# Performance work log

Measured on AMD Instinct MI355X. Metric: run time of the kernel, lower is better.

The kernel has to match this reference:

```python
import jax, jax.numpy as jnp
import numpy as np

EPS = 1e-5  # torch BatchNorm2d default eps

def _bn(x, gamma, beta):
    # training-mode batch statistics over (N,H,W), per channel (biased variance)
    mean = jnp.mean(x, axis=(0, 2, 3), keepdims=True)
    var = jnp.var(x, axis=(0, 2, 3), keepdims=True)
    return gamma[None, :, None, None] * (x - mean) * jax.lax.rsqrt(var + EPS) + beta[None, :, None, None]

def _conv1x1(x, w, b):
    # (B,C,H,W) x (O,C) -> (B,O,H,W)
    return jnp.einsum('bchw,oc->bohw', x, w) + b[None, :, None, None]

def _maxpool2(x):
    B, C, H, W = x.shape
    return x.reshape(B, C, H // 2, 2, W // 2, 2).max(axis=(3, 5))

def setup_inputs() -> dict:
    key = jax.random.key(0)
    ks = jax.random.split(key, 5)
    B, C, H, W = 16, 256, 56, 56
    Ci, Cg = C // 8, C // 4
    def kaiming(k, o, i):
        return jax.random.normal(k, (o, i), jnp.float32) * np.float32(np.sqrt(2.0 / i))
    return {
        'x': jax.random.normal(ks[0], (B, C, H, W), jnp.float32),
        'bn1_gamma': jnp.ones((C,), jnp.float32),
        'bn1_beta': jnp.zeros((C,), jnp.float32),
        'w_g': kaiming(ks[1], Cg, C), 'b_g': jnp.zeros((Cg,), jnp.float32),
        'w_theta': kaiming(ks[2], Ci, C), 'b_theta': jnp.zeros((Ci,), jnp.float32),
        'w_phi': kaiming(ks[3], Ci, C), 'b_phi': jnp.zeros((Ci,), jnp.float32),
        'bn2_gamma': jnp.ones((Cg,), jnp.float32),
        'bn2_beta': jnp.zeros((Cg,), jnp.float32),
        'w_z': kaiming(ks[4], C, Cg), 'b_z': jnp.zeros((C,), jnp.float32),
    }

def reference(x, bn1_gamma, bn1_beta, w_g, b_g, w_theta, b_theta, w_phi, b_phi, bn2_gamma, bn2_beta, w_z, b_z):
    identity = x
    B, C, H, W = x.shape
    xa = jax.nn.relu(_bn(x, bn1_gamma, bn1_beta))
    g_x = _maxpool2(_conv1x1(xa, w_g, b_g))        # (B,Cg,H/2,W/2)
    phi_x = _maxpool2(_conv1x1(xa, w_phi, b_phi))  # (B,Ci,H/2,W/2)
    theta_x = _conv1x1(xa, w_theta, b_theta)       # (B,Ci,H,W)
    Cg = g_x.shape[1]
    Ci = theta_x.shape[1]
    Np = g_x.shape[2] * g_x.shape[3]               # subsampled positions (H/2*W/2)
    g_x = g_x.reshape(B, Cg, Np).transpose(0, 2, 1)      # (B,Np,Cg)
    phi_x = phi_x.reshape(B, Ci, Np)                     # (B,Ci,Np)
    theta_x = theta_x.reshape(B, Ci, H * W).transpose(0, 2, 1)  # (B,HW,Ci)
    f_div_C = jnp.einsum('bnc,bcm->bnm', theta_x, phi_x) / Np   # (B,HW,Np)
    y = jnp.einsum('bnm,bmc->bnc', f_div_C, g_x)                # (B,HW,Cg)
    y = y.transpose(0, 2, 1).reshape(B, Cg, H, W)
    w_y = _conv1x1(jax.nn.relu(_bn(y, bn2_gamma, bn2_beta)), w_z, b_z)
    return w_y + identity
```

## Files before the change

### kernel.cpp

```cpp
#include <hip/hip_runtime.h>
#include <hip/hip_bf16.h>

#define BB 16
#define CC 256
#define HWN 3136
#define NCG 64
#define NCI 32
#define NPP 784

typedef __attribute__((ext_vector_type(8))) short short8;
typedef __attribute__((ext_vector_type(4))) float floatx4;

__device__ __forceinline__ unsigned short f2bf(float f) {
    union { __hip_bfloat16 h; unsigned short u; } cv;
    cv.h = __float2bfloat16(f);
    return cv.u;
}
__device__ __forceinline__ float bf2f(unsigned short u) {
    return __uint_as_float(((unsigned)u) << 16);
}

__global__ __launch_bounds__(256) void k_prep(const float* __restrict__ w_t,
                                              const float* __restrict__ w_p,
                                              const float* __restrict__ w_g,
                                              const float* __restrict__ w_z,
                                              unsigned short* __restrict__ wcat,
                                              unsigned short* __restrict__ wzb,
                                              unsigned short* __restrict__ pool,
                                              float* __restrict__ accs) {
    int o = blockIdx.x;
    int c = threadIdx.x;
    const float* src = (o < 32) ? (w_t + o * CC)
                      : (o < 64) ? (w_p + (o - 32) * CC)
                                 : (w_g + (o - 64) * CC);
    wcat[o * CC + c] = f2bf(src[c]);
    {
        int r = o * 2 + (c >> 7);
        int kk = c & 127;
        if (kk < 72)
            wzb[r * 72 + kk] = (kk < 64) ? f2bf(w_z[r * 64 + kk]) : (unsigned short)0;
    }
    if (o < 96) {
        int b = c >> 4, kk = c & 15;
        pool[((size_t)(b * 96 + o)) * 800 + 784 + kk] = 0;
    }
    if (o == 0) {
        for (int i = c; i < 1152; i += 256) accs[i] = 0.f;
    }
}

__global__ __launch_bounds__(256) void k_bn1a(const float* __restrict__ x,
                                              float* __restrict__ acc) {
    int blk = blockIdx.x;
    int c = blk & (CC - 1);
    const float4* p = (const float4*)(x + (size_t)blk * HWN);
    int tid = threadIdx.x;
    float s = 0.f, q = 0.f;
    #pragma unroll
    for (int i = tid; i < 784; i += 256) {
        float4 v = p[i];
        s += v.x + v.y + v.z + v.w;
        q += v.x * v.x + v.y * v.y + v.z * v.z + v.w * v.w;
    }
    #pragma unroll
    for (int off = 32; off > 0; off >>= 1) {
        s += __shfl_down(s, off);
        q += __shfl_down(q, off);
    }
    __shared__ float sh[8];
    int wid = tid >> 6, lane = tid & 63;
    if (lane == 0) { sh[wid] = s; sh[4 + wid] = q; }
    __syncthreads();
    if (tid == 0) {
        atomicAdd(&acc[c], sh[0] + sh[1] + sh[2] + sh[3]);
        atomicAdd(&acc[CC + c], sh[4] + sh[5] + sh[6] + sh[7]);
    }
}

__global__ __launch_bounds__(256) void k_conv1(const float* __restrict__ x,
                                               const unsigned short* __restrict__ wcat,
                                               const float* __restrict__ bn1acc,
                                               const float* __restrict__ gamma,
                                               const float* __restrict__ beta,
                                               const float* __restrict__ b_g,
                                               const float* __restrict__ b_t,
                                               const float* __restrict__ b_p,
                                               unsigned short* __restrict__ th,
                                               unsigned short* __restrict__ pool,
                                               float* __restrict__ T1g) {
    int b  = blockIdx.y;
    int bx = blockIdx.x;
    int hw0 = bx * 112;
    int tid = threadIdx.x;
    int wv = tid >> 6, ln = tid & 63;
    int col = ln & 15, quad = ln >> 4;

    __shared__ unsigned short smem[128 * 120];
    unsigned short* As = smem;
    unsigned short* Bs = smem + 4096;
    __shared__ float ab_s[512];
    __shared__ float bias_s[128];

    {
        const float inv = 1.0f / (BB * HWN);
        float mean = bn1acc[tid] * inv;
        float var  = bn1acc[CC + tid] * inv - mean * mean;
        float a = gamma[tid] * rsqrtf(var + 1e-5f);
        ab_s[tid] = a;
        ab_s[CC + tid] = beta[tid] - mean * a;
    }
    if (tid < 128) {
        int o = tid;
        bias_s[o] = (o < 32) ? b_t[o] : (o < 64) ? b_p[o - 32] : b_g[o - 64];
    }
    __syncthreads();

    floatx4 acc[2][7];
    #pragma unroll
    for (int mt = 0; mt < 2; ++mt)
        for (int nt = 0; nt < 7; ++nt)
            acc[mt][nt] = (floatx4){0.f, 0.f, 0.f, 0.f};

    int p   = tid & 15;
    int hwq = tid >> 4;
    const float* xb = x + (size_t)(b * CC) * HWN + hw0;
    bool q1 = (hwq + 16) < 28;

    float4 pv0[2], pv1[2];
    {
        int c0 = 2 * p;
        pv0[0] = *(const float4*)(xb + (size_t)c0 * HWN + hwq * 4);
        pv1[0] = *(const float4*)(xb + (size_t)(c0 + 1) * HWN + hwq * 4);
        if (q1) {
            pv0[1] = *(const float4*)(xb + (size_t)c0 * HWN + (hwq + 16) * 4);
            pv1[1] = *(const float4*)(xb + (size_t)(c0 + 1) * HWN + (hwq + 16) * 4);
        }
    }

    for (int k0 = 0; k0 < CC; k0 += 32) {
        #pragma unroll
        for (int i = 0; i < 2; ++i) {
            int row = wv * 32 + i * 16 + (ln >> 2);
            int q   = ln & 3;
            const unsigned short* gp = wcat + row * CC + k0 + q * 8;
            __builtin_amdgcn_global_load_lds(
                (const __attribute__((address_space(1))) unsigned int*)gp,
                (__attribute__((address_space(3))) unsigned int*)&As[(wv * 2 + i) * 512],
                16, 0, 0);
        }
        {
            int c0 = k0 + 2 * p;
            float a0 = ab_s[c0],     d0 = ab_s[CC + c0];
            float a1 = ab_s[c0 + 1], d1 = ab_s[CC + c0 + 1];
            unsigned int* bw = (unsigned int*)Bs;
            #pragma unroll
            for (int t = 0; t < 2; ++t) {
                if (t == 0 || q1) {
                    int qi = hwq + 16 * t;
                    float4 v0 = pv0[t], v1 = pv1[t];
                    float r0[4] = { fmaxf(fmaf(a0, v0.x, d0), 0.f), fmaxf(fmaf(a0, v0.y, d0), 0.f),
                                    fmaxf(fmaf(a0, v0.z, d0), 0.f), fmaxf(fmaf(a0, v0.w, d0), 0.f) };
                    float r1[4] = { fmaxf(fmaf(a1, v1.x, d1), 0.f), fmaxf(fmaf(a1, v1.y, d1), 0.f),
                                    fmaxf(fmaf(a1, v1.z, d1), 0.f), fmaxf(fmaf(a1, v1.w, d1), 0.f) };
                    #pragma unroll
                    for (int i = 0; i < 4; ++i) {
                        unsigned int w = (unsigned int)f2bf(r0[i]) | ((unsigned int)f2bf(r1[i]) << 16);
                        bw[(qi * 4 + i) * 16 + p] = w;
                    }
                }
            }
        }
        if (k0 + 32 < CC) {
            int c0 = k0 + 32 + 2 * p;
            pv0[0] = *(const float4*)(xb + (size_t)c0 * HWN + hwq * 4);
            pv1[0] = *(const float4*)(xb + (size_t)(c0 + 1) * HWN + hwq * 4);
            if (q1) {
                pv0[1] = *(const float4*)(xb + (size_t)c0 * HWN + (hwq + 16) * 4);
                pv1[1] = *(const float4*)(xb + (size_t)(c0 + 1) * HWN + (hwq + 16) * 4);
            }
        }
        __syncthreads();

        short8 af0 = *(const short8*)&As[(wv * 32 +      col) * 32 + quad * 8];
        short8 af1 = *(const short8*)&As[(wv * 32 + 16 + col) * 32 + quad * 8];
        #pragma unroll
        for (int nt = 0; nt < 7; ++nt) {
            short8 bf = *(const short8*)&Bs[(nt * 16 + col) * 32 + quad * 8];
            acc[0][nt] = __builtin_amdgcn_mfma_f32_16x16x32_bf16(af0, bf, acc[0][nt], 0, 0, 0);
            acc[1][nt] = __builtin_amdgcn_mfma_f32_16x16x32_bf16(af1, bf, acc[1][nt], 0, 0, 0);
        }
        __syncthreads();
    }

    unsigned short* Ct = smem;
    #pragma unroll
    for (int mt = 0; mt < 2; ++mt) {
        int obase = wv * 32 + mt * 16 + quad * 4;
        #pragma unroll
        for (int r = 0; r < 4; ++r) {
            float bias = bias_s[obase + r];
            #pragma unroll
            for (int nt = 0; nt < 7; ++nt)
                Ct[(obase + r) * 120 + nt * 16 + col] = f2bf(acc[mt][nt][r] + bias);
        }
    }
    __syncthreads();

    #pragma unroll
    for (int i = 0; i < 4; ++i) {
        int e = tid + i * 256;
        if (e < 896) {
            int ch = e / 28, c4 = e - ch * 28;
            ushort4 v = *(const ushort4*)&Ct[ch * 120 + c4 * 4];
            *(ushort4*)&th[((size_t)(b * NCI + ch)) * HWN + hw0 + c4 * 4] = v;
        }
    }
    {
        int row = tid >> 3;
        int seg = tid & 7;
        float s = 0.f;
        #pragma unroll
        for (int j = 0; j < 14; ++j) s += bf2f(Ct[row * 120 + seg * 14 + j]);
        s += __shfl_down(s, 4);
        s += __shfl_down(s, 2);
        s += __shfl_down(s, 1);
        if (seg == 0) atomicAdd(&T1g[b * NCI + row], s);
    }
    #pragma unroll
    for (int i = 0; i < 11; ++i) {
        int e = tid + i * 256;
        if (e < 2688) {
            int ch = e / 28, m = e - ch * 28;
            const unsigned short* r0p = &Ct[(32 + ch) * 120 + 2 * m];
            float v = fmaxf(fmaxf(bf2f(r0p[0]), bf2f(r0p[1])),
                            fmaxf(bf2f(r0p[56]), bf2f(r0p[57])));
            pool[((size_t)(b * 96 + ch)) * 800 + bx * 28 + m] = f2bf(v);
        }
    }
}

__global__ __launch_bounds__(512) void k_sgemm(const unsigned short* __restrict__ pool,
                                               const unsigned short* __restrict__ th,
                                               const float* __restrict__ T1g,
                                               unsigned short* __restrict__ Sg,
                                               float* __restrict__ bn2acc) {
    int b = blockIdx.x;
    int tid = threadIdx.x;
    int wv = tid >> 6, ln = tid & 63;
    int col = ln & 15, quad = ln >> 4;
    __shared__ float Sred[4 * 2048];
    __shared__ float Gred[4 * 1024];
    __shared__ float T1s[32];
    __shared__ float shs[64], shq[64];

    if (tid < 64) { shs[tid] = 0.f; shq[tid] = 0.f; }
    if (tid < 32) T1s[tid] = T1g[b * NCI + tid];

    if (wv < 4) {
        const unsigned short* gbase = pool + ((size_t)(b * 96 + 32)) * 800;
        const unsigned short* pbase = pool + ((size_t)(b * 96)) * 800;
        floatx4 acc[4][2];
        #pragma unroll
        for (int mt = 0; mt < 4; ++mt)
            for (int nt = 0; nt < 2; ++nt)
                acc[mt][nt] = (floatx4){0.f, 0.f, 0.f, 0.f};
        for (int s = wv; s < 25; s += 4) {
            int k0 = s * 32;
            short8 af[4], bfr[2];
            #pragma unroll
            for (int mt = 0; mt < 4; ++mt)
                af[mt] = *(const short8*)&gbase[(mt * 16 + col) * 800 + k0 + quad * 8];
            #pragma unroll
            for (int nt = 0; nt < 2; ++nt)
                bfr[nt] = *(const short8*)&pbase[(nt * 16 + col) * 800 + k0 + quad * 8];
            #pragma unroll
            for (int mt = 0; mt < 4; ++mt)
                #pragma unroll
                for (int nt = 0; nt < 2; ++nt)
                    acc[mt][nt] = __builtin_amdgcn_mfma_f32_16x16x32_bf16(af[mt], bfr[nt], acc[mt][nt], 0, 0, 0);
        }
        #pragma unroll
        for (int mt = 0; mt < 4; ++mt)
            for (int nt = 0; nt < 2; ++nt)
                for (int r = 0; r < 4; ++r) {
                    int cg = mt * 16 + quad * 4 + r;
                    int ci = nt * 16 + col;
                    Sred[wv * 2048 + cg * 32 + ci] = acc[mt][nt][r];
                }
    } else {
        int gw = wv - 4;
        const unsigned short* tb = th + (size_t)(b * NCI) * HWN;
        floatx4 ga[2][2];
        #pragma unroll
        for (int m = 0; m < 2; ++m)
            for (int n = 0; n < 2; ++n)
                ga[m][n] = (floatx4){0.f, 0.f, 0.f, 0.f};
        for (int t = gw; t < 98; t += 4) {
            int k0 = t * 32;
            short8 a0 = *(const short8*)&tb[(size_t)col * HWN + k0 + quad * 8];
            short8 a1 = *(const short8*)&tb[(size_t)(16 + col) * HWN + k0 + quad * 8];
            ga[0][0] = __builtin_amdgcn_mfma_f32_16x16x32_bf16(a0, a0, ga[0][0], 0, 0, 0);
            ga[0][1] = __builtin_amdgcn_mfma_f32_16x16x32_bf16(a0, a1, ga[0][1], 0, 0, 0);
            ga[1][0] = __builtin_amdgcn_mfma_f32_16x16x32_bf16(a1, a0, ga[1][0], 0, 0, 0);
            ga[1][1] = __builtin_amdgcn_mfma_f32_16x16x32_bf16(a1, a1, ga[1][1], 0, 0, 0);
        }
        #pragma unroll
        for (int m = 0; m < 2; ++m)
            for (int n = 0; n < 2; ++n)
                for (int r = 0; r < 4; ++r)
                    Gred[gw * 1024 + (m * 16 + quad * 4 + r) * 32 + n * 16 + col] = ga[m][n][r];
    }
    __syncthreads();

    for (int idx = tid; idx < 2048; idx += 512) {
        float s = Sred[idx] + Sred[2048 + idx] + Sred[4096 + idx] + Sred[6144 + idx];
        int cg = idx >> 5, ci = idx & 31;
        unsigned short h = f2bf(s * (1.0f / NPP));
        Sg[(size_t)b * 2560 + cg * 40 + ci] = h;
        Sred[idx] = bf2f(h);
    }
    for (int idx = tid; idx < 1024; idx += 512) {
        Gred[idx] = Gred[idx] + Gred[1024 + idx] + Gred[2048 + idx] + Gred[3072 + idx];
    }
    __syncthreads();

    {
        int cg = tid & 63, part = tid >> 6;
        float sum = 0.f, sq = 0.f;
        #pragma unroll
        for (int i = 0; i < 4; ++i) {
            int ci = part * 4 + i;
            float sv = Sred[cg * 32 + ci];
            sum += sv * T1s[ci];
            float t = 0.f;
            #pragma unroll
            for (int cj = 0; cj < 32; ++cj)
                t += Gred[ci * 32 + cj] * Sred[cg * 32 + cj];
            sq += sv * t;
        }
        atomicAdd(&shs[cg], sum);
        atomicAdd(&shq[cg], sq);
    }
    __syncthreads();
    if (tid < 64) {
        atomicAdd(&bn2acc[tid], shs[tid]);
        atomicAdd(&bn2acc[64 + tid], shq[tid]);
    }
}

__global__ __launch_bounds__(256) void k_convz(const unsigned short* __restrict__ th,
                                               const unsigned short* __restrict__ Sg,
                                               const unsigned short* __restrict__ wzb,
                                               const float* __restrict__ bn2acc,
                                               const float* __restrict__ gamma,
                                               const float* __restrict__ beta,
                                               const float* __restrict__ b_z,
                                               const float* __restrict__ x,
                                               float* __restrict__ out) {
    int b = blockIdx.y;
    int hw0 = blockIdx.x * 64;
    int coh = blockIdx.z * 128;
    int tid = threadIdx.x;
    int wv = tid >> 6, ln = tid & 63;
    int col = ln & 15, quad = ln >> 4;

    __shared__ unsigned short Wl[128 * 72];
    __shared__ unsigned short TS[5120];
    __shared__ float ab2_s[128];
    unsigned short* Tt = TS;
    unsigned short* St = TS + 2560;
    unsigned short* Yt = TS;

    for (int j = wv; j < 18; j += 4) {
        const unsigned short* gp = wzb + coh * 72 + j * 512 + ln * 8;
        __builtin_amdgcn_global_load_lds(
            (const __attribute__((address_space(1))) unsigned int*)gp,
            (__attribute__((address_space(3))) unsigned int*)&Wl[j * 512],
            16, 0, 0);
    }
    if (tid < 64) {
        const float inv = 1.0f / (BB * HWN);
        float mean = bn2acc[tid] * inv;
        float var  = bn2acc[64 + tid] * inv - mean * mean;
        float a = gamma[tid] * rsqrtf(var + 1e-5f);
        ab2_s[tid] = a;
        ab2_s[64 + tid] = beta[tid] - mean * a;
    }
    {
        const unsigned int* sgw = (const unsigned int*)(Sg + (size_t)b * 2560);
        unsigned int* stw = (unsigned int*)St;
        for (int i = tid; i < 1280; i += 256) stw[i] = sgw[i];
    }
    {
        int p2 = tid & 15, hwq = tid >> 4;
        int c0 = 2 * p2;
        const unsigned short* tb = th + (size_t)(b * NCI) * HWN + hw0 + hwq * 4;
        ushort4 v0 = *(const ushort4*)(tb + (size_t)c0 * HWN);
        ushort4 v1 = *(const ushort4*)(tb + (size_t)(c0 + 1) * HWN);
        unsigned int* tw = (unsigned int*)Tt;
        tw[(hwq * 4 + 0) * 20 + p2] = (unsigned)v0.x | ((unsigned)v1.x << 16);
        tw[(hwq * 4 + 1) * 20 + p2] = (unsigned)v0.y | ((unsigned)v1.y << 16);
        tw[(hwq * 4 + 2) * 20 + p2] = (unsigned)v0.z | ((unsigned)v1.z << 16);
        tw[(hwq * 4 + 3) * 20 + p2] = (unsigned)v0.w | ((unsigned)v1.w << 16);
    }
    __syncthreads();

    short8 afy = *(const short8*)&Tt[(wv * 16 + col) * 40 + quad * 8];
    floatx4 yacc[4];
    #pragma unroll
    for (int nt = 0; nt < 4; ++nt) {
        short8 bf = *(const short8*)&St[(nt * 16 + col) * 40 + quad * 8];
        floatx4 z = (floatx4){0.f, 0.f, 0.f, 0.f};
        yacc[nt] = __builtin_amdgcn_mfma_f32_16x16x32_bf16(afy, bf, z, 0, 0, 0);
    }
    __syncthreads();

    #pragma unroll
    for (int nt = 0; nt < 4; ++nt) {
        int cg = nt * 16 + col;
        float a = ab2_s[cg], d = ab2_s[64 + cg];
        #pragma unroll
        for (int r = 0; r < 4; ++r) {
            int hwl = wv * 16 + quad * 4 + r;
            Yt[hwl * 72 + cg] = f2bf(fmaxf(fmaf(a, yacc[nt][r], d), 0.f));
        }
    }
    __syncthreads();

    floatx4 acc[8];
    #pragma unroll
    for (int nt = 0; nt < 8; ++nt) acc[nt] = (floatx4){0.f, 0.f, 0.f, 0.f};

    #pragma unroll
    for (int kk = 0; kk < 2; ++kk) {
        short8 afm = *(const short8*)&Yt[(wv * 16 + col) * 72 + kk * 32 + quad * 8];
        #pragma unroll
        for (int nt = 0; nt < 8; ++nt) {
            short8 bf = *(const short8*)&Wl[(nt * 16 + col) * 72 + kk * 32 + quad * 8];
            acc[nt] = __builtin_amdgcn_mfma_f32_16x16x32_bf16(afm, bf, acc[nt], 0, 0, 0);
        }
    }

    #pragma unroll
    for (int nt = 0; nt < 8; ++nt) {
        int co = coh + nt * 16 + col;
        size_t base = ((size_t)(b * CC + co)) * HWN + hw0 + wv * 16 + quad * 4;
        float4 xv = *(const float4*)&x[base];
        float bz = b_z[co];
        float4 r = make_float4(acc[nt][0] + bz + xv.x, acc[nt][1] + bz + xv.y,
                               acc[nt][2] + bz + xv.z, acc[nt][3] + bz + xv.w);
        *(float4*)&out[base] = r;
    }
}

extern "C" void kernel_launch(void* const* d_in, const int* in_sizes, int n_in,
                              void* d_out, int out_size, void* d_ws, size_t ws_size,
                              hipStream_t stream) {
    (void)in_sizes; (void)n_in; (void)out_size; (void)ws_size;
    const float* x   = (const float*)d_in[0];
    const float* g1  = (const float*)d_in[1];
    const float* b1  = (const float*)d_in[2];
    const float* w_g = (const float*)d_in[3];
    const float* b_g = (const float*)d_in[4];
    const float* w_t = (const float*)d_in[5];
    const float* b_t = (const float*)d_in[6];
    const float* w_p = (const float*)d_in[7];
    const float* b_p = (const float*)d_in[8];
    const float* g2  = (const float*)d_in[9];
    const float* b2  = (const float*)d_in[10];
    const float* w_z = (const float*)d_in[11];
    const float* b_z = (const float*)d_in[12];
    float* out = (float*)d_out;

    float* ws     = (float*)d_ws;
    float* bn1acc = ws;
    float* bn2acc = ws + 512;
    float* T1g    = ws + 640;
    unsigned short* wcat = (unsigned short*)(ws + 1152);
    unsigned short* wzb  = (unsigned short*)(ws + 17536);
    unsigned short* th   = (unsigned short*)(ws + 26752);
    unsigned short* pool = (unsigned short*)(ws + 829568);
    unsigned short* Sg   = (unsigned short*)(ws + 1443968);

    k_prep  <<<dim3(128),        dim3(256), 0, stream>>>(w_t, w_p, w_g, w_z, wcat, wzb, pool, ws);
    k_bn1a  <<<dim3(BB * CC),    dim3(256), 0, stream>>>(x, bn1acc);
    k_conv1 <<<dim3(28, BB),     dim3(256), 0, stream>>>(x, wcat, bn1acc, g1, b1, b_g, b_t, b_p, th, pool, T1g);
    k_sgemm <<<dim3(BB),         dim3(512), 0, stream>>>(pool, th, T1g, Sg, bn2acc);
    k_convz <<<dim3(49, BB, 2),  dim3(256), 0, stream>>>(th, Sg, wzb, bn2acc, g2, b2, b_z, x, out);
}
```

Measured before the change: 174.6 us.

## Merge prep and BN1 kernels, move theta Gram into conv1, widen convz

Merges the weight-prep and BN1-statistics kernels into one launch, and replaces the BN1 atomics with per-(batch,channel) partial sums that conv1 reduces itself. The theta Gram matrix is now computed from the conv1 output tile in shared memory and atomically accumulated, so k_sgemm no longer rereads theta from global memory and uses all 8 waves for the S GEMM. It also moves a barrier in conv1's k-loop ahead of the next prefetch, and makes convz compute all 256 output channels per block instead of splitting them over two blocks. The trade-offs are extra atomics in conv1, more registers and shared memory in convz, and fewer blocks in the convz grid.

```diff
diff --git a/kernel.cpp b/kernel.cpp
--- a/kernel.cpp
+++ b/kernel.cpp
@@ -20,43 +20,42 @@
     return __uint_as_float(((unsigned)u) << 16);
 }
 
-__global__ __launch_bounds__(256) void k_prep(const float* __restrict__ w_t,
+__global__ __launch_bounds__(256) void k_head(const float* __restrict__ x,
+                                              const float* __restrict__ w_t,
                                               const float* __restrict__ w_p,
                                               const float* __restrict__ w_g,
                                               const float* __restrict__ w_z,
                                               unsigned short* __restrict__ wcat,
                                               unsigned short* __restrict__ wzb,
                                               unsigned short* __restrict__ pool,
-                                              float* __restrict__ accs) {
-    int o = blockIdx.x;
+                                              float* __restrict__ zacc,
+                                              float* __restrict__ bn1part) {
+    int blk = blockIdx.x;
     int c = threadIdx.x;
-    const float* src = (o < 32) ? (w_t + o * CC)
-                      : (o < 64) ? (w_p + (o - 32) * CC)
-                                 : (w_g + (o - 64) * CC);
-    wcat[o * CC + c] = f2bf(src[c]);
-    {
-        int r = o * 2 + (c >> 7);
-        int kk = c & 127;
-        if (kk < 72)
-            wzb[r * 72 + kk] = (kk < 64) ? f2bf(w_z[r * 64 + kk]) : (unsigned short)0;
-    }
-    if (o < 96) {
-        int b = c >> 4, kk = c & 15;
-        pool[((size_t)(b * 96 + o)) * 800 + 784 + kk] = 0;
-    }
-    if (o == 0) {
-        for (int i = c; i < 1152; i += 256) accs[i] = 0.f;
-    }
-}
-
-__global__ __launch_bounds__(256) void k_bn1a(const float* __restrict__ x,
-                                              float* __restrict__ acc) {
-    int blk = blockIdx.x;
-    int c = blk & (CC - 1);
-    const float4* p = (const float4*)(x + (size_t)blk * HWN);
-    int tid = threadIdx.x;
+    if (blk < 128) {
+        int o = blk;
+        const float* src = (o < 32) ? (w_t + o * CC)
+                          : (o < 64) ? (w_p + (o - 32) * CC)
+                                     : (w_g + (o - 64) * CC);
+        wcat[o * CC + c] = f2bf(src[c]);
+        {
+            int r = o * 2 + (c >> 7);
+            int kk = c & 127;
+            if (kk < 72)
+                wzb[r * 72 + kk] = (kk < 64) ? f2bf(w_z[r * 64 + kk]) : (unsigned short)0;
+        }
+        if (o < 96) {
+            int b = c >> 4, kk = c & 15;
+            pool[((size_t)(b * 96 + o)) * 800 + 784 + kk] = 0;
+        }
+        int idx = o * 256 + c;
+        if (idx < 17024) zacc[idx] = 0.f;
+        return;
+    }
+    int bc = blk - 128;
+    const float4* p = (const float4*)(x + (size_t)bc * HWN);
+    int tid = c;
     float s = 0.f, q = 0.f;
-    #pragma unroll
     for (int i = tid; i < 784; i += 256) {
         float4 v = p[i];
         s += v.x + v.y + v.z + v.w;
@@ -67,19 +66,17 @@
         s += __shfl_down(s, off);
         q += __shfl_down(q, off);
     }
-    __shared__ float sh[8];
+    __shared__ float sh[16];
     int wid = tid >> 6, lane = tid & 63;
-    if (lane == 0) { sh[wid] = s; sh[4 + wid] = q; }
-    __syncthreads();
-    if (tid == 0) {
-        atomicAdd(&acc[c], sh[0] + sh[1] + sh[2] + sh[3]);
-        atomicAdd(&acc[CC + c], sh[4] + sh[5] + sh[6] + sh[7]);
-    }
+    if (lane == 0) { sh[wid] = s; sh[8 + wid] = q; }
+    __syncthreads();
+    if (tid == 0) bn1part[bc]        = sh[0] + sh[1] + sh[2] + sh[3];
+    if (tid == 1) bn1part[4096 + bc] = sh[8] + sh[9] + sh[10] + sh[11];
 }
 
 __global__ __launch_bounds__(256) void k_conv1(const float* __restrict__ x,
                                                const unsigned short* __restrict__ wcat,
-                                               const float* __restrict__ bn1acc,
+                                               const float* __restrict__ bn1part,
                                                const float* __restrict__ gamma,
                                                const float* __restrict__ beta,
                                                const float* __restrict__ b_g,
@@ -87,7 +84,8 @@
                                                const float* __restrict__ b_p,
                                                unsigned short* __restrict__ th,
                                                unsigned short* __restrict__ pool,
-                                               float* __restrict__ T1g) {
+                                               float* __restrict__ T1g,
+                                               float* __restrict__ Gg) {
     int b  = blockIdx.y;
     int bx = blockIdx.x;
     int hw0 = bx * 112;
@@ -103,8 +101,14 @@
 
     {
         const float inv = 1.0f / (BB * HWN);
-        float mean = bn1acc[tid] * inv;
-        float var  = bn1acc[CC + tid] * inv - mean * mean;
+        float s = 0.f, q = 0.f;
+        #pragma unroll
+        for (int b2 = 0; b2 < BB; ++b2) {
+            s += bn1part[b2 * 256 + tid];
+            q += bn1part[4096 + b2 * 256 + tid];
+        }
+        float mean = s * inv;
+        float var  = q * inv - mean * mean;
         float a = gamma[tid] * rsqrtf(var + 1e-5f);
         ab_s[tid] = a;
         ab_s[CC + tid] = beta[tid] - mean * a;
@@ -170,6 +174,8 @@
                 }
             }
         }
+        __syncthreads();
+
         if (k0 + 32 < CC) {
             int c0 = k0 + 32 + 2 * p;
             pv0[0] = *(const float4*)(xb + (size_t)c0 * HWN + hwq * 4);
@@ -179,7 +185,6 @@
                 pv1[1] = *(const float4*)(xb + (size_t)(c0 + 1) * HWN + (hwq + 16) * 4);
             }
         }
-        __syncthreads();
 
         short8 af0 = *(const short8*)&As[(wv * 32 +      col) * 32 + quad * 8];
         short8 af1 = *(const short8*)&As[(wv * 32 + 16 + col) * 32 + quad * 8];
@@ -225,6 +230,25 @@
         s += __shfl_down(s, 2);
         s += __shfl_down(s, 1);
         if (seg == 0) atomicAdd(&T1g[b * NCI + row], s);
+    }
+    {
+        int m = wv >> 1, n = wv & 1;
+        floatx4 g = (floatx4){0.f, 0.f, 0.f, 0.f};
+        short8 z8 = (short8){0, 0, 0, 0, 0, 0, 0, 0};
+        #pragma unroll
+        for (int ks = 0; ks < 4; ++ks) {
+            short8 ga, gb;
+            if (ks < 3 || quad < 2) {
+                ga = *(const short8*)&Ct[(m * 16 + col) * 120 + ks * 32 + quad * 8];
+                gb = *(const short8*)&Ct[(n * 16 + col) * 120 + ks * 32 + quad * 8];
+            } else {
+                ga = z8; gb = z8;
+            }
+            g = __builtin_amdgcn_mfma_f32_16x16x32_bf16(ga, gb, g, 0, 0, 0);
+        }
+        float* gg = Gg + b * 1024 + (m * 16 + quad * 4) * 32 + n * 16 + col;
+        #pragma unroll
+        for (int r = 0; r < 4; ++r) atomicAdd(&gg[r * 32], g[r]);
     }
     #pragma unroll
     for (int i = 0; i < 11; ++i) {
@@ -240,87 +264,63 @@
 }
 
 __global__ __launch_bounds__(512) void k_sgemm(const unsigned short* __restrict__ pool,
-                                               const unsigned short* __restrict__ th,
                                                const float* __restrict__ T1g,
+                                               const float* __restrict__ Gg,
                                                unsigned short* __restrict__ Sg,
                                                float* __restrict__ bn2acc) {
     int b = blockIdx.x;
     int tid = threadIdx.x;
     int wv = tid >> 6, ln = tid & 63;
     int col = ln & 15, quad = ln >> 4;
-    __shared__ float Sred[4 * 2048];
-    __shared__ float Gred[4 * 1024];
+    __shared__ float Sred[8 * 2048];
+    __shared__ float Gred[1024];
     __shared__ float T1s[32];
     __shared__ float shs[64], shq[64];
 
     if (tid < 64) { shs[tid] = 0.f; shq[tid] = 0.f; }
     if (tid < 32) T1s[tid] = T1g[b * NCI + tid];
-
-    if (wv < 4) {
-        const unsigned short* gbase = pool + ((size_t)(b * 96 + 32)) * 800;
-        const unsigned short* pbase = pool + ((size_t)(b * 96)) * 800;
-        floatx4 acc[4][2];
+    for (int idx = tid; idx < 1024; idx += 512) Gred[idx] = Gg[b * 1024 + idx];
+
+    const unsigned short* gbase = pool + ((size_t)(b * 96 + 32)) * 800;
+    const unsigned short* pbase = pool + ((size_t)(b * 96)) * 800;
+    floatx4 acc[4][2];
+    #pragma unroll
+    for (int mt = 0; mt < 4; ++mt)
+        for (int nt = 0; nt < 2; ++nt)
+            acc[mt][nt] = (floatx4){0.f, 0.f, 0.f, 0.f};
+    for (int s = wv; s < 25; s += 8) {
+        int k0 = s * 32;
+        short8 af[4], bfr[2];
         #pragma unroll
         for (int mt = 0; mt < 4; ++mt)
-            for (int nt = 0; nt < 2; ++nt)
-                acc[mt][nt] = (floatx4){0.f, 0.f, 0.f, 0.f};
-        for (int s = wv; s < 25; s += 4) {
-            int k0 = s * 32;
-            short8 af[4], bfr[2];
-            #pragma unroll
-            for (int mt = 0; mt < 4; ++mt)
-                af[mt] = *(const short8*)&gbase[(mt * 16 + col) * 800 + k0 + quad * 8];
+            af[mt] = *(const short8*)&gbase[(mt * 16 + col) * 800 + k0 + quad * 8];
+        #pragma unroll
+        for (int nt = 0; nt < 2; ++nt)
+            bfr[nt] = *(const short8*)&pbase[(nt * 16 + col) * 800 + k0 + quad * 8];
+        #pragma unroll
+        for (int mt = 0; mt < 4; ++mt)
             #pragma unroll
             for (int nt = 0; nt < 2; ++nt)
-                bfr[nt] = *(const short8*)&pbase[(nt * 16 + col) * 800 + k0 + quad * 8];
-            #pragma unroll
-            for (int mt = 0; mt < 4; ++mt)
-                #pragma unroll
-                for (int nt = 0; nt < 2; ++nt)
-                    acc[mt][nt] = __builtin_amdgcn_mfma_f32_16x16x32_bf16(af[mt], bfr[nt], acc[mt][nt], 0, 0, 0);
-        }
-        #pragma unroll
-        for (int mt = 0; mt < 4; ++mt)
-            for (int nt = 0; nt < 2; ++nt)
-                for (int r = 0; r < 4; ++r) {
-                    int cg = mt * 16 + quad * 4 + r;
-                    int ci = nt * 16 + col;
-                    Sred[wv * 2048 + cg * 32 + ci] = acc[mt][nt][r];
-                }
-    } else {
-        int gw = wv - 4;
-        const unsigned short* tb = th + (size_t)(b * NCI) * HWN;
-        floatx4 ga[2][2];
-        #pragma unroll
-        for (int m = 0; m < 2; ++m)
-            for (int n = 0; n < 2; ++n)
-                ga[m][n] = (floatx4){0.f, 0.f, 0.f, 0.f};
-        for (int t = gw; t < 98; t += 4) {
-            int k0 = t * 32;
-            short8 a0 = *(const short8*)&tb[(size_t)col * HWN + k0 + quad * 8];
-            short8 a1 = *(const short8*)&tb[(size_t)(16 + col) * HWN + k0 + quad * 8];
-            ga[0][0] = __builtin_amdgcn_mfma_f32_16x16x32_bf16(a0, a0, ga[0][0], 0, 0, 0);
-            ga[0][1] = __builtin_amdgcn_mfma_f32_16x16x32_bf16(a0, a1, ga[0][1], 0, 0, 0);
-            ga[1][0] = __builtin_amdgcn_mfma_f32_16x16x32_bf16(a1, a0, ga[1][0], 0, 0, 0);
-            ga[1][1] = __builtin_amdgcn_mfma_f32_16x16x32_bf16(a1, a1, ga[1][1], 0, 0, 0);
-        }
-        #pragma unroll
-        for (int m = 0; m < 2; ++m)
-            for (int n = 0; n < 2; ++n)
-                for (int r = 0; r < 4; ++r)
-                    Gred[gw * 1024 + (m * 16 + quad * 4 + r) * 32 + n * 16 + col] = ga[m][n][r];
-    }
+                acc[mt][nt] = __builtin_amdgcn_mfma_f32_16x16x32_bf16(af[mt], bfr[nt], acc[mt][nt], 0, 0, 0);
+    }
+    #pragma unroll
+    for (int mt = 0; mt < 4; ++mt)
+        for (int nt = 0; nt < 2; ++nt)
+            for (int r = 0; r < 4; ++r) {
+                int cg = mt * 16 + quad * 4 + r;
+                int ci = nt * 16 + col;
+                Sred[wv * 2048 + cg * 32 + ci] = acc[mt][nt][r];
+            }
     __syncthreads();
 
     for (int idx = tid; idx < 2048; idx += 512) {
-        float s = Sred[idx] + Sred[2048 + idx] + Sred[4096 + idx] + Sred[6144 + idx];
+        float s = 0.f;
+        #pragma unroll
+        for (int w = 0; w < 8; ++w) s += Sred[w * 2048 + idx];
         int cg = idx >> 5, ci = idx & 31;
         unsigned short h = f2bf(s * (1.0f / NPP));
         Sg[(size_t)b * 2560 + cg * 40 + ci] = h;
         Sred[idx] = bf2f(h);
-    }
-    for (int idx = tid; idx < 1024; idx += 512) {
-        Gred[idx] = Gred[idx] + Gred[1024 + idx] + Gred[2048 + idx] + Gred[3072 + idx];
     }
     __syncthreads();
 
@@ -359,20 +359,19 @@
                                                float* __restrict__ out) {
     int b = blockIdx.y;
     int hw0 = blockIdx.x * 64;
-    int coh = blockIdx.z * 128;
     int tid = threadIdx.x;
     int wv = tid >> 6, ln = tid & 63;
     int col = ln & 15, quad = ln >> 4;
 
-    __shared__ unsigned short Wl[128 * 72];
+    __shared__ unsigned short Wl[256 * 72];
     __shared__ unsigned short TS[5120];
     __shared__ float ab2_s[128];
     unsigned short* Tt = TS;
     unsigned short* St = TS + 2560;
     unsigned short* Yt = TS;
 
-    for (int j = wv; j < 18; j += 4) {
-        const unsigned short* gp = wzb + coh * 72 + j * 512 + ln * 8;
+    for (int j = wv; j < 36; j += 4) {
+        const unsigned short* gp = wzb + j * 512 + ln * 8;
         __builtin_amdgcn_global_load_lds(
             (const __attribute__((address_space(1))) unsigned int*)gp,
             (__attribute__((address_space(3))) unsigned int*)&Wl[j * 512],
@@ -427,23 +426,23 @@
     }
     __syncthreads();
 
-    floatx4 acc[8];
-    #pragma unroll
-    for (int nt = 0; nt < 8; ++nt) acc[nt] = (floatx4){0.f, 0.f, 0.f, 0.f};
+    floatx4 acc[16];
+    #pragma unroll
+    for (int nt = 0; nt < 16; ++nt) acc[nt] = (floatx4){0.f, 0.f, 0.f, 0.f};
 
     #pragma unroll
     for (int kk = 0; kk < 2; ++kk) {
         short8 afm = *(const short8*)&Yt[(wv * 16 + col) * 72 + kk * 32 + quad * 8];
         #pragma unroll
-        for (int nt = 0; nt < 8; ++nt) {
+        for (int nt = 0; nt < 16; ++nt) {
             short8 bf = *(const short8*)&Wl[(nt * 16 + col) * 72 + kk * 32 + quad * 8];
             acc[nt] = __builtin_amdgcn_mfma_f32_16x16x32_bf16(afm, bf, acc[nt], 0, 0, 0);
         }
     }
 
     #pragma unroll
-    for (int nt = 0; nt < 8; ++nt) {
-        int co = coh + nt * 16 + col;
+    for (int nt = 0; nt < 16; ++nt) {
+        int co = nt * 16 + col;
         size_t base = ((size_t)(b * CC + co)) * HWN + hw0 + wv * 16 + quad * 4;
         float4 xv = *(const float4*)&x[base];
         float bz = b_z[co];
@@ -472,19 +471,20 @@
     const float* b_z = (const float*)d_in[12];
     float* out = (float*)d_out;
 
-    float* ws     = (float*)d_ws;
-    float* bn1acc = ws;
-    float* bn2acc = ws + 512;
-    float* T1g    = ws + 640;
-    unsigned short* wcat = (unsigned short*)(ws + 1152);
-    unsigned short* wzb  = (unsigned short*)(ws + 17536);
-    unsigned short* th   = (unsigned short*)(ws + 26752);
-    unsigned short* pool = (unsigned short*)(ws + 829568);
-    unsigned short* Sg   = (unsigned short*)(ws + 1443968);
-
-    k_prep  <<<dim3(128),        dim3(256), 0, stream>>>(w_t, w_p, w_g, w_z, wcat, wzb, pool, ws);
-    k_bn1a  <<<dim3(BB * CC),    dim3(256), 0, stream>>>(x, bn1acc);
-    k_conv1 <<<dim3(28, BB),     dim3(256), 0, stream>>>(x, wcat, bn1acc, g1, b1, b_g, b_t, b_p, th, pool, T1g);
-    k_sgemm <<<dim3(BB),         dim3(512), 0, stream>>>(pool, th, T1g, Sg, bn2acc);
-    k_convz <<<dim3(49, BB, 2),  dim3(256), 0, stream>>>(th, Sg, wzb, bn2acc, g2, b2, b_z, x, out);
-}
+    float* ws      = (float*)d_ws;
+    float* bn1part = ws;
+    float* zacc    = ws + 8192;
+    float* bn2acc  = ws + 8192;
+    float* T1g     = ws + 8320;
+    float* Gg      = ws + 8832;
+    unsigned short* wcat = (unsigned short*)(ws + 25216);
+    unsigned short* wzb  = (unsigned short*)(ws + 41600);
+    unsigned short* th   = (unsigned short*)(ws + 50816);
+    unsigned short* pool = (unsigned short*)(ws + 853632);
+    unsigned short* Sg   = (unsigned short*)(ws + 1468032);
+
+    k_head  <<<dim3(4224),     dim3(256), 0, stream>>>(x, w_t, w_p, w_g, w_z, wcat, wzb, pool, zacc, bn1part);
+    k_conv1 <<<dim3(28, BB),   dim3(256), 0, stream>>>(x, wcat, bn1part, g1, b1, b_g, b_t, b_p, th, pool, T1g, Gg);
+    k_sgemm <<<dim3(BB),       dim3(512), 0, stream>>>(pool, T1g, Gg, Sg, bn2acc);
+    k_convz <<<dim3(49, BB),   dim3(256), 0, stream>>>(th, Sg, wzb, bn2acc, g2, b2, b_z, x, out);
+}
```

Result: faster. 170.5 us (-2.3%).
